# Optimization experiments

Hardware: AMD Instinct MI355X
Metric: run time of the kernel (lower is better)

## Reference

```python
import jax, jax.numpy as jnp
import numpy as np

# Dims: N tokens, top_k K, E experts, d_model D, expert hidden H
N, K, E, D, H = 4096, 2, 8, 1024, 1024


def setup_inputs() -> dict:
    key = jax.random.key(0)
    k1, k2, k3, k4, k5, k6 = jax.random.split(key, 6)
    x = jax.random.normal(k1, (N, D), dtype=jnp.float32)
    expert_indices = jax.random.randint(k2, (N, K), 0, E, dtype=jnp.int32)
    ew = jax.random.uniform(k3, (N, K), dtype=jnp.float32)
    expert_weights = ew / ew.sum(-1, keepdims=True)  # router probs over top-k
    # histogram consistent with expert_indices (computed by the router in the real model)
    batch_size_per_expert = jnp.bincount(expert_indices.reshape(-1), length=E).astype(jnp.int32)
    w1 = jax.random.normal(k4, (E, D, H), dtype=jnp.float32) * (D ** -0.5)
    w3 = jax.random.normal(k5, (E, D, H), dtype=jnp.float32) * (D ** -0.5)
    w2 = jax.random.normal(k6, (E, H, D), dtype=jnp.float32) * (H ** -0.5)
    return {
        "x": x,
        "expert_weights": expert_weights,
        "expert_indices": expert_indices,
        "batch_size_per_expert": batch_size_per_expert,
        "w1": w1,
        "w2": w2,
        "w3": w3,
    }


def reference(x, expert_weights, expert_indices, batch_size_per_expert, w1, w2, w3):
    """Dropless MoE: sort token-copies by expert, grouped-GEMM SwiGLU, unpermute+combine."""
    nk = N * K
    flat_idx = expert_indices.reshape(nk)               # (N*K,)
    order = jnp.argsort(flat_idx)                        # stable sort -> permutation into expert order
    x_perm = x[order // K]                               # (N*K, D) gather source token per copy
    gs = batch_size_per_expert.astype(jnp.int32)         # grouped-GEMM group sizes, sums to N*K
    # per-expert SwiGLU MLP via grouped GEMM (rows of x_perm are contiguous per expert)
    h = jax.nn.silu(jax.lax.ragged_dot(x_perm, w1, gs)) * jax.lax.ragged_dot(x_perm, w3, gs)  # (N*K, H)
    out_perm = jax.lax.ragged_dot(h, w2, gs)             # (N*K, D)
    # unpermute: scatter rows back to original (token, k) order
    out_flat = jnp.zeros_like(x_perm).at[order].set(out_perm)  # (N*K, D)
    # weighted combine over top-k copies
    out = jnp.einsum("nk,nkd->nd", expert_weights, out_flat.reshape(N, K, D))
    return out
```

## Files before the change

kernel.cpp:

```cpp
#include <hip/hip_runtime.h>
#include <hip/hip_bf16.h>
#include <stdint.h>

#define N_TOK   4096
#define TOPK    2
#define N_EXP   8
#define D_MODEL 1024
#define H_DIM   1024
#define NK      (N_TOK * TOPK)
#define MAX_TILES 72

typedef __attribute__((ext_vector_type(8))) short bf16x8;
typedef __attribute__((ext_vector_type(4))) float f32x4;
typedef unsigned short bfbits;

__device__ inline bfbits f2bf_bits(float f) {
  union { float f; unsigned int u; } v; v.f = f;
  unsigned int r = v.u + 0x7FFFu + ((v.u >> 16) & 1u);
  return (bfbits)(r >> 16);
}

__device__ inline void glds16(const bfbits* g, bfbits* l) {
  __builtin_amdgcn_global_load_lds(
      (const __attribute__((address_space(1))) void*)g,
      (__attribute__((address_space(3))) void*)l, 16, 0, 0);
}

__global__ void prep_bucket_kernel(const int* __restrict__ bspe, const int* __restrict__ eidx,
                                   int* __restrict__ meta, int* __restrict__ row_src,
                                   int* __restrict__ pos_of) {
  __shared__ int sm[162];
  __shared__ int scnt[N_EXP];
  int t = threadIdx.x;
  if (t == 0) {
    int acc = 0, nt = 0;
    for (int e = 0; e < N_EXP; e++) {
      sm[e] = acc;
      sm[9 + e] = 0;
      int g = bspe[e];
      for (int tt = 0; tt * 128 < g; tt++) {
        sm[18 + nt] = e;
        sm[90 + nt] = acc + tt * 128;
        nt++;
      }
      acc += g;
    }
    sm[8] = acc;
    sm[17] = nt;
    for (int i = nt; i < MAX_TILES; i++) { sm[18 + i] = 0; sm[90 + i] = 0; }
  }
  if (t < N_EXP) scnt[t] = 0;
  __syncthreads();
  for (int i = t; i < NK; i += 256) {
    int e = eidx[i];
    int p = sm[e] + atomicAdd(&scnt[e], 1);
    row_src[p] = i;
    pos_of[i] = p;
  }
  if (t < 162) meta[t] = sm[t];
}

__global__ void convx_kernel(const float4* __restrict__ x, ushort4* __restrict__ xb) {
  int i = blockIdx.x * 256 + threadIdx.x;
  float4 v = x[i];
  ushort4 o;
  o.x = f2bf_bits(v.x); o.y = f2bf_bits(v.y);
  o.z = f2bf_bits(v.z); o.w = f2bf_bits(v.w);
  xb[i] = o;
}

__global__ void wtrans_kernel(const float* __restrict__ w1, const float* __restrict__ w2,
                              const float* __restrict__ w3,
                              bfbits* __restrict__ w1t, bfbits* __restrict__ w2t,
                              bfbits* __restrict__ w3t) {
  int z = blockIdx.z;
  const size_t MAT = (size_t)1024 * 1024;
  const float* src; bfbits* dst;
  if (z < 8)       { src = w1 + (size_t)z * MAT;        dst = w1t + (size_t)z * MAT; }
  else if (z < 16) { src = w3 + (size_t)(z - 8) * MAT;  dst = w3t + (size_t)(z - 8) * MAT; }
  else             { src = w2 + (size_t)(z - 16) * MAT; dst = w2t + (size_t)(z - 16) * MAT; }
  __shared__ bfbits tl[64][65];
  int tid = threadIdx.x;
  int r0 = blockIdx.y * 64, c0 = blockIdx.x * 64;
  for (int it = 0; it < 4; it++) {
    int r = (tid >> 4) + it * 16;
    int c = (tid & 15) * 4;
    float4 v = *(const float4*)&src[(size_t)(r0 + r) * 1024 + c0 + c];
    tl[r][c + 0] = f2bf_bits(v.x); tl[r][c + 1] = f2bf_bits(v.y);
    tl[r][c + 2] = f2bf_bits(v.z); tl[r][c + 3] = f2bf_bits(v.w);
  }
  __syncthreads();
  for (int it = 0; it < 4; it++) {
    int o = (tid >> 4) + it * 16;
    int r4 = (tid & 15) * 4;
    ushort4 v;
    v.x = tl[r4 + 0][o]; v.y = tl[r4 + 1][o];
    v.z = tl[r4 + 2][o]; v.w = tl[r4 + 3][o];
    *(ushort4*)&dst[(size_t)(c0 + o) * 1024 + r0 + r4] = v;
  }
}

__global__ __launch_bounds__(256, 3) void gemm_swiglu_kernel(
    const bfbits* __restrict__ xb, const bfbits* __restrict__ w1t,
    const bfbits* __restrict__ w3t, const int* __restrict__ row_src,
    const int* __restrict__ meta, bfbits* __restrict__ hb) {
  int nt = meta[17];
  int bt = blockIdx.y;
  if (bt >= nt) return;
  int e = meta[18 + bt];
  int row0 = meta[90 + bt];
  int rows_end = meta[e + 1];
  int n0 = blockIdx.x * 64;

  __shared__ __align__(16) bfbits As[128 * 32];
  __shared__ __align__(16) bfbits B1s[64 * 32];
  __shared__ __align__(16) bfbits B3s[64 * 32];

  int tid = threadIdx.x, lane = tid & 63, wv = tid >> 6;
  int g = (lane & 3) ^ ((lane >> 3) & 3);
  int rlo = lane >> 2;

  const bfbits* gp[4]; bfbits* lp[4];
  for (int j = 0; j < 4; j++) {
    int s = wv * 4 + j;
    if (s < 8) {
      int gr = row0 + s * 16 + rlo;
      int tok = row_src[(gr < rows_end) ? gr : row0] >> 1;
      gp[j] = xb + (size_t)tok * D_MODEL + g * 8;
      lp[j] = As + s * 512;
    } else if (s < 12) {
      int b = s - 8;
      gp[j] = w1t + ((size_t)e * H_DIM + n0 + b * 16 + rlo) * D_MODEL + g * 8;
      lp[j] = B1s + b * 512;
    } else {
      int b = s - 12;
      gp[j] = w3t + ((size_t)e * H_DIM + n0 + b * 16 + rlo) * D_MODEL + g * 8;
      lp[j] = B3s + b * 512;
    }
  }

  const f32x4 fzero = {0.f, 0.f, 0.f, 0.f};
  f32x4 accg[4][2], accu[4][2];
  for (int i = 0; i < 4; i++)
    for (int j = 0; j < 2; j++) { accg[i][j] = fzero; accu[i][j] = fzero; }

  int mw = (wv & 1) * 64, nwv = (wv >> 1) * 32;
  int qd = lane >> 4, lr = lane & 15;
  int slot = (qd ^ ((lr >> 1) & 3)) << 3;

  for (int kk = 0; kk < D_MODEL / 32; kk++) {
    int ko = kk * 32;
    glds16(gp[0] + ko, lp[0]);
    glds16(gp[1] + ko, lp[1]);
    glds16(gp[2] + ko, lp[2]);
    glds16(gp[3] + ko, lp[3]);
    __syncthreads();
    bf16x8 af[4], b1f[2], b3f[2];
    for (int mi = 0; mi < 4; mi++)
      af[mi] = *(const bf16x8*)&As[(mw + mi * 16 + lr) * 32 + slot];
    for (int ni = 0; ni < 2; ni++) {
      b1f[ni] = *(const bf16x8*)&B1s[(nwv + ni * 16 + lr) * 32 + slot];
      b3f[ni] = *(const bf16x8*)&B3s[(nwv + ni * 16 + lr) * 32 + slot];
    }
    for (int mi = 0; mi < 4; mi++)
      for (int ni = 0; ni < 2; ni++) {
        accg[mi][ni] = __builtin_amdgcn_mfma_f32_16x16x32_bf16(af[mi], b1f[ni], accg[mi][ni], 0, 0, 0);
        accu[mi][ni] = __builtin_amdgcn_mfma_f32_16x16x32_bf16(af[mi], b3f[ni], accu[mi][ni], 0, 0, 0);
      }
    __syncthreads();
  }

  for (int mi = 0; mi < 4; mi++) {
    int rbase = row0 + mw + mi * 16 + qd * 4;
    for (int r = 0; r < 4; r++) {
      int grow = rbase + r;
      if (grow < rows_end) {
        for (int ni = 0; ni < 2; ni++) {
          float gg = accg[mi][ni][r], u = accu[mi][ni][r];
          float h = gg / (1.f + __expf(-gg)) * u;
          hb[(size_t)grow * H_DIM + n0 + nwv + ni * 16 + lr] = f2bf_bits(h);
        }
      }
    }
  }
}

__global__ __launch_bounds__(256, 4) void gemm_out_kernel(
    const bfbits* __restrict__ hb, const bfbits* __restrict__ w2t,
    const int* __restrict__ meta, float* __restrict__ out_perm) {
  int nt = meta[17];
  int bt = blockIdx.y;
  if (bt >= nt) return;
  int e = meta[18 + bt];
  int row0 = meta[90 + bt];
  int rows_end = meta[e + 1];
  int n0 = blockIdx.x * 64;

  __shared__ __align__(16) bfbits As[128 * 32];
  __shared__ __align__(16) bfbits Bs[64 * 32];

  int tid = threadIdx.x, lane = tid & 63, wv = tid >> 6;
  int g = (lane & 3) ^ ((lane >> 3) & 3);
  int rlo = lane >> 2;

  const bfbits* gp[3]; bfbits* lp[3];
  for (int j = 0; j < 3; j++) {
    int s = wv * 3 + j;
    if (s < 8) {
      int gr = row0 + s * 16 + rlo;
      int sr = (gr < rows_end) ? gr : row0;
      gp[j] = hb + (size_t)sr * H_DIM + g * 8;
      lp[j] = As + s * 512;
    } else {
      int b = s - 8;
      gp[j] = w2t + ((size_t)e * D_MODEL + n0 + b * 16 + rlo) * H_DIM + g * 8;
      lp[j] = Bs + b * 512;
    }
  }

  const f32x4 fzero = {0.f, 0.f, 0.f, 0.f};
  f32x4 acc[4][2];
  for (int i = 0; i < 4; i++)
    for (int j = 0; j < 2; j++) acc[i][j] = fzero;

  int mw = (wv & 1) * 64, nwv = (wv >> 1) * 32;
  int qd = lane >> 4, lr = lane & 15;
  int slot = (qd ^ ((lr >> 1) & 3)) << 3;

  for (int kk = 0; kk < H_DIM / 32; kk++) {
    int ko = kk * 32;
    glds16(gp[0] + ko, lp[0]);
    glds16(gp[1] + ko, lp[1]);
    glds16(gp[2] + ko, lp[2]);
    __syncthreads();
    bf16x8 af[4], bfr[2];
    for (int mi = 0; mi < 4; mi++)
      af[mi] = *(const bf16x8*)&As[(mw + mi * 16 + lr) * 32 + slot];
    for (int ni = 0; ni < 2; ni++)
      bfr[ni] = *(const bf16x8*)&Bs[(nwv + ni * 16 + lr) * 32 + slot];
    for (int mi = 0; mi < 4; mi++)
      for (int ni = 0; ni < 2; ni++)
        acc[mi][ni] = __builtin_amdgcn_mfma_f32_16x16x32_bf16(af[mi], bfr[ni], acc[mi][ni], 0, 0, 0);
    __syncthreads();
  }

  for (int mi = 0; mi < 4; mi++) {
    int rbase = row0 + mw + mi * 16 + qd * 4;
    for (int r = 0; r < 4; r++) {
      int grow = rbase + r;
      if (grow < rows_end) {
        for (int ni = 0; ni < 2; ni++)
          out_perm[(size_t)grow * D_MODEL + n0 + nwv + ni * 16 + lr] = acc[mi][ni][r];
      }
    }
  }
}

__global__ void combine_kernel(const float4* __restrict__ out_perm,
                               const int* __restrict__ pos_of,
                               const float* __restrict__ ew, float4* __restrict__ out) {
  int i = blockIdx.x * 256 + threadIdx.x;
  int tok = i >> 8;
  int col = i & 255;
  int p0 = pos_of[2 * tok], p1 = pos_of[2 * tok + 1];
  float w0 = ew[2 * tok], w1 = ew[2 * tok + 1];
  float4 a = out_perm[(size_t)p0 * 256 + col];
  float4 b = out_perm[(size_t)p1 * 256 + col];
  float4 o;
  o.x = w0 * a.x + w1 * b.x;
  o.y = w0 * a.y + w1 * b.y;
  o.z = w0 * a.z + w1 * b.z;
  o.w = w0 * a.w + w1 * b.w;
  out[i] = o;
}

extern "C" void kernel_launch(void* const* d_in, const int* in_sizes, int n_in,
                              void* d_out, int out_size, void* d_ws, size_t ws_size,
                              hipStream_t stream) {
  const float* x  = (const float*)d_in[0];
  const float* ew = (const float*)d_in[1];
  const int* eidx = (const int*)d_in[2];
  const int* bspe = (const int*)d_in[3];
  const float* w1 = (const float*)d_in[4];
  const float* w2 = (const float*)d_in[5];
  const float* w3 = (const float*)d_in[6];
  float* out = (float*)d_out;

  char* ws = (char*)d_ws;
  const size_t MB = 1024 * 1024;
  bfbits* w1t   = (bfbits*)(ws);
  bfbits* w3t   = (bfbits*)(ws + 16 * MB);
  bfbits* w2t   = (bfbits*)(ws + 32 * MB);
  bfbits* xb    = (bfbits*)(ws + 48 * MB);
  bfbits* hb    = (bfbits*)(ws + 56 * MB);
  float* out_perm = (float*)(ws);
  int* row_src  = (int*)(ws + 72 * MB);
  int* pos_of   = (int*)(ws + 72 * MB + 32 * 1024);
  int* meta     = (int*)(ws + 72 * MB + 64 * 1024);

  prep_bucket_kernel<<<1, 256, 0, stream>>>(bspe, eidx, meta, row_src, pos_of);
  convx_kernel<<<(N_TOK * D_MODEL / 4) / 256, 256, 0, stream>>>((const float4*)x, (ushort4*)xb);
  wtrans_kernel<<<dim3(16, 16, 24), 256, 0, stream>>>(w1, w2, w3, w1t, w2t, w3t);
  gemm_swiglu_kernel<<<dim3(H_DIM / 64, MAX_TILES), 256, 0, stream>>>(
      xb, w1t, w3t, row_src, meta, hb);
  gemm_out_kernel<<<dim3(D_MODEL / 64, MAX_TILES), 256, 0, stream>>>(
      hb, w2t, meta, out_perm);
  combine_kernel<<<(N_TOK * D_MODEL / 4) / 256, 256, 0, stream>>>(
      (const float4*)out_perm, pos_of, ew, (float4*)out);
}
```

Baseline: 283.1 us.

## Merge prep kernels, double GEMM K-step, and store expert output in bf16

Combines weight transpose, x conversion and bucketing into one launch. Both grouped GEMMs now stage 64-wide K slices with an 8-way XOR swizzle, halving barrier count per K. The per-copy expert output is written as bf16 and widened in the combine kernel, halving that traffic. Tail-row clamping was dropped, so the last tile may read row_src entries beyond valid rows and gather unrelated tokens (masked on store, but indices past NK read adjacent buffer memory).

Measured after the change: 248.6 us. 12.2% less time.

```diff
diff --git a/kernel.cpp b/kernel.cpp
--- a/kernel.cpp
+++ b/kernel.cpp
@@ -19,6 +19,10 @@
   unsigned int r = v.u + 0x7FFFu + ((v.u >> 16) & 1u);
   return (bfbits)(r >> 16);
 }
+__device__ inline float bf2f(unsigned short u) {
+  union { unsigned int u; float f; } v; v.u = ((unsigned int)u) << 16;
+  return v.f;
+}
 
 __device__ inline void glds16(const bfbits* g, bfbits* l) {
   __builtin_amdgcn_global_load_lds(
@@ -26,77 +30,76 @@
       (__attribute__((address_space(3))) void*)l, 16, 0, 0);
 }
 
-__global__ void prep_bucket_kernel(const int* __restrict__ bspe, const int* __restrict__ eidx,
-                                   int* __restrict__ meta, int* __restrict__ row_src,
-                                   int* __restrict__ pos_of) {
-  __shared__ int sm[162];
-  __shared__ int scnt[N_EXP];
-  int t = threadIdx.x;
-  if (t == 0) {
-    int acc = 0, nt = 0;
-    for (int e = 0; e < N_EXP; e++) {
-      sm[e] = acc;
-      sm[9 + e] = 0;
-      int g = bspe[e];
-      for (int tt = 0; tt * 128 < g; tt++) {
-        sm[18 + nt] = e;
-        sm[90 + nt] = acc + tt * 128;
-        nt++;
+__global__ void prepass_kernel(const float* __restrict__ x, const int* __restrict__ eidx,
+                               const int* __restrict__ bspe,
+                               const float* __restrict__ w1, const float* __restrict__ w2,
+                               const float* __restrict__ w3,
+                               bfbits* __restrict__ w1t, bfbits* __restrict__ w2t,
+                               bfbits* __restrict__ w3t, bfbits* __restrict__ xb,
+                               int* __restrict__ meta, int* __restrict__ row_src,
+                               int* __restrict__ pos_of) {
+  int z = blockIdx.z;
+  int tid = threadIdx.x;
+  if (z < 24) {
+    const size_t MAT = (size_t)1024 * 1024;
+    const float* src; bfbits* dst;
+    if (z < 8)       { src = w1 + (size_t)z * MAT;        dst = w1t + (size_t)z * MAT; }
+    else if (z < 16) { src = w3 + (size_t)(z - 8) * MAT;  dst = w3t + (size_t)(z - 8) * MAT; }
+    else             { src = w2 + (size_t)(z - 16) * MAT; dst = w2t + (size_t)(z - 16) * MAT; }
+    __shared__ bfbits tl[64][65];
+    int r0 = blockIdx.y * 64, c0 = blockIdx.x * 64;
+    for (int it = 0; it < 4; it++) {
+      int r = (tid >> 4) + it * 16;
+      int c = (tid & 15) * 4;
+      float4 v = *(const float4*)&src[(size_t)(r0 + r) * 1024 + c0 + c];
+      tl[r][c + 0] = f2bf_bits(v.x); tl[r][c + 1] = f2bf_bits(v.y);
+      tl[r][c + 2] = f2bf_bits(v.z); tl[r][c + 3] = f2bf_bits(v.w);
+    }
+    __syncthreads();
+    for (int it = 0; it < 4; it++) {
+      int o = (tid >> 4) + it * 16;
+      int r4 = (tid & 15) * 4;
+      ushort4 v;
+      v.x = tl[r4 + 0][o]; v.y = tl[r4 + 1][o];
+      v.z = tl[r4 + 2][o]; v.w = tl[r4 + 3][o];
+      *(ushort4*)&dst[(size_t)(c0 + o) * 1024 + r0 + r4] = v;
+    }
+  } else if (z < 40) {
+    int i = ((z - 24) * 256 + blockIdx.y * 16 + blockIdx.x) * 256 + tid;
+    float4 v = ((const float4*)x)[i];
+    ushort4 o;
+    o.x = f2bf_bits(v.x); o.y = f2bf_bits(v.y);
+    o.z = f2bf_bits(v.z); o.w = f2bf_bits(v.w);
+    ((ushort4*)xb)[i] = o;
+  } else {
+    if (blockIdx.x != 0 || blockIdx.y != 0) return;
+    __shared__ int sm[162];
+    __shared__ int scnt[N_EXP];
+    if (tid == 0) {
+      int acc = 0, nt = 0;
+      for (int e = 0; e < N_EXP; e++) {
+        sm[e] = acc;
+        int g = bspe[e];
+        for (int tt = 0; tt * 128 < g; tt++) {
+          sm[18 + nt] = e;
+          sm[90 + nt] = acc + tt * 128;
+          nt++;
+        }
+        acc += g;
       }
-      acc += g;
-    }
-    sm[8] = acc;
-    sm[17] = nt;
-    for (int i = nt; i < MAX_TILES; i++) { sm[18 + i] = 0; sm[90 + i] = 0; }
-  }
-  if (t < N_EXP) scnt[t] = 0;
-  __syncthreads();
-  for (int i = t; i < NK; i += 256) {
-    int e = eidx[i];
-    int p = sm[e] + atomicAdd(&scnt[e], 1);
-    row_src[p] = i;
-    pos_of[i] = p;
-  }
-  if (t < 162) meta[t] = sm[t];
-}
-
-__global__ void convx_kernel(const float4* __restrict__ x, ushort4* __restrict__ xb) {
-  int i = blockIdx.x * 256 + threadIdx.x;
-  float4 v = x[i];
-  ushort4 o;
-  o.x = f2bf_bits(v.x); o.y = f2bf_bits(v.y);
-  o.z = f2bf_bits(v.z); o.w = f2bf_bits(v.w);
-  xb[i] = o;
-}
-
-__global__ void wtrans_kernel(const float* __restrict__ w1, const float* __restrict__ w2,
-                              const float* __restrict__ w3,
-                              bfbits* __restrict__ w1t, bfbits* __restrict__ w2t,
-                              bfbits* __restrict__ w3t) {
-  int z = blockIdx.z;
-  const size_t MAT = (size_t)1024 * 1024;
-  const float* src; bfbits* dst;
-  if (z < 8)       { src = w1 + (size_t)z * MAT;        dst = w1t + (size_t)z * MAT; }
-  else if (z < 16) { src = w3 + (size_t)(z - 8) * MAT;  dst = w3t + (size_t)(z - 8) * MAT; }
-  else             { src = w2 + (size_t)(z - 16) * MAT; dst = w2t + (size_t)(z - 16) * MAT; }
-  __shared__ bfbits tl[64][65];
-  int tid = threadIdx.x;
-  int r0 = blockIdx.y * 64, c0 = blockIdx.x * 64;
-  for (int it = 0; it < 4; it++) {
-    int r = (tid >> 4) + it * 16;
-    int c = (tid & 15) * 4;
-    float4 v = *(const float4*)&src[(size_t)(r0 + r) * 1024 + c0 + c];
-    tl[r][c + 0] = f2bf_bits(v.x); tl[r][c + 1] = f2bf_bits(v.y);
-    tl[r][c + 2] = f2bf_bits(v.z); tl[r][c + 3] = f2bf_bits(v.w);
-  }
-  __syncthreads();
-  for (int it = 0; it < 4; it++) {
-    int o = (tid >> 4) + it * 16;
-    int r4 = (tid & 15) * 4;
-    ushort4 v;
-    v.x = tl[r4 + 0][o]; v.y = tl[r4 + 1][o];
-    v.z = tl[r4 + 2][o]; v.w = tl[r4 + 3][o];
-    *(ushort4*)&dst[(size_t)(c0 + o) * 1024 + r0 + r4] = v;
+      sm[8] = acc;
+      sm[17] = nt;
+      for (int i = nt; i < MAX_TILES; i++) { sm[18 + i] = 0; sm[90 + i] = 0; }
+    }
+    if (tid < N_EXP) scnt[tid] = 0;
+    __syncthreads();
+    for (int i = tid; i < NK; i += 256) {
+      int e = eidx[i];
+      int p = sm[e] + atomicAdd(&scnt[e], 1);
+      row_src[p] = i;
+      pos_of[i] = p;
+    }
+    if (tid < 162) meta[tid] = sm[tid];
   }
 }
 
@@ -112,29 +115,28 @@
   int rows_end = meta[e + 1];
   int n0 = blockIdx.x * 64;
 
-  __shared__ __align__(16) bfbits As[128 * 32];
-  __shared__ __align__(16) bfbits B1s[64 * 32];
-  __shared__ __align__(16) bfbits B3s[64 * 32];
+  __shared__ __align__(16) bfbits As[128 * 64];
+  __shared__ __align__(16) bfbits B1s[64 * 64];
+  __shared__ __align__(16) bfbits B3s[64 * 64];
 
   int tid = threadIdx.x, lane = tid & 63, wv = tid >> 6;
-  int g = (lane & 3) ^ ((lane >> 3) & 3);
-  int rlo = lane >> 2;
-
-  const bfbits* gp[4]; bfbits* lp[4];
-  for (int j = 0; j < 4; j++) {
-    int s = wv * 4 + j;
-    if (s < 8) {
-      int gr = row0 + s * 16 + rlo;
-      int tok = row_src[(gr < rows_end) ? gr : row0] >> 1;
-      gp[j] = xb + (size_t)tok * D_MODEL + g * 8;
+  int r8 = lane >> 3, jl = lane & 7;
+  int jg = jl ^ r8;
+
+  const bfbits* gp[8]; bfbits* lp[8];
+  for (int j = 0; j < 8; j++) {
+    int s = wv * 8 + j;
+    if (s < 16) {
+      int tok = row_src[row0 + s * 8 + r8] >> 1;
+      gp[j] = xb + (size_t)tok * D_MODEL + jg * 8;
       lp[j] = As + s * 512;
-    } else if (s < 12) {
-      int b = s - 8;
-      gp[j] = w1t + ((size_t)e * H_DIM + n0 + b * 16 + rlo) * D_MODEL + g * 8;
+    } else if (s < 24) {
+      int b = s - 16;
+      gp[j] = w1t + ((size_t)e * H_DIM + n0 + b * 8 + r8) * D_MODEL + jg * 8;
       lp[j] = B1s + b * 512;
     } else {
-      int b = s - 12;
-      gp[j] = w3t + ((size_t)e * H_DIM + n0 + b * 16 + rlo) * D_MODEL + g * 8;
+      int b = s - 24;
+      gp[j] = w3t + ((size_t)e * H_DIM + n0 + b * 8 + r8) * D_MODEL + jg * 8;
       lp[j] = B3s + b * 512;
     }
   }
@@ -145,28 +147,27 @@
     for (int j = 0; j < 2; j++) { accg[i][j] = fzero; accu[i][j] = fzero; }
 
   int mw = (wv & 1) * 64, nwv = (wv >> 1) * 32;
-  int qd = lane >> 4, lr = lane & 15;
-  int slot = (qd ^ ((lr >> 1) & 3)) << 3;
-
-  for (int kk = 0; kk < D_MODEL / 32; kk++) {
-    int ko = kk * 32;
-    glds16(gp[0] + ko, lp[0]);
-    glds16(gp[1] + ko, lp[1]);
-    glds16(gp[2] + ko, lp[2]);
-    glds16(gp[3] + ko, lp[3]);
-    __syncthreads();
-    bf16x8 af[4], b1f[2], b3f[2];
-    for (int mi = 0; mi < 4; mi++)
-      af[mi] = *(const bf16x8*)&As[(mw + mi * 16 + lr) * 32 + slot];
-    for (int ni = 0; ni < 2; ni++) {
-      b1f[ni] = *(const bf16x8*)&B1s[(nwv + ni * 16 + lr) * 32 + slot];
-      b3f[ni] = *(const bf16x8*)&B3s[(nwv + ni * 16 + lr) * 32 + slot];
-    }
-    for (int mi = 0; mi < 4; mi++)
+  int qd = lane >> 4, lr = lane & 15, lr7 = lr & 7;
+
+  for (int kk = 0; kk < D_MODEL / 64; kk++) {
+    int ko = kk * 64;
+    for (int j = 0; j < 8; j++) glds16(gp[j] + ko, lp[j]);
+    __syncthreads();
+    for (int ks = 0; ks < 2; ks++) {
+      int sb = ((ks * 4 + qd) ^ lr7) << 3;
+      bf16x8 af[4], b1f[2], b3f[2];
+      for (int mi = 0; mi < 4; mi++)
+        af[mi] = *(const bf16x8*)&As[(mw + mi * 16 + lr) * 64 + sb];
       for (int ni = 0; ni < 2; ni++) {
-        accg[mi][ni] = __builtin_amdgcn_mfma_f32_16x16x32_bf16(af[mi], b1f[ni], accg[mi][ni], 0, 0, 0);
-        accu[mi][ni] = __builtin_amdgcn_mfma_f32_16x16x32_bf16(af[mi], b3f[ni], accu[mi][ni], 0, 0, 0);
+        b1f[ni] = *(const bf16x8*)&B1s[(nwv + ni * 16 + lr) * 64 + sb];
+        b3f[ni] = *(const bf16x8*)&B3s[(nwv + ni * 16 + lr) * 64 + sb];
       }
+      for (int mi = 0; mi < 4; mi++)
+        for (int ni = 0; ni < 2; ni++) {
+          accg[mi][ni] = __builtin_amdgcn_mfma_f32_16x16x32_bf16(af[mi], b1f[ni], accg[mi][ni], 0, 0, 0);
+          accu[mi][ni] = __builtin_amdgcn_mfma_f32_16x16x32_bf16(af[mi], b3f[ni], accu[mi][ni], 0, 0, 0);
+        }
+    }
     __syncthreads();
   }
 
@@ -187,7 +188,7 @@
 
 __global__ __launch_bounds__(256, 4) void gemm_out_kernel(
     const bfbits* __restrict__ hb, const bfbits* __restrict__ w2t,
-    const int* __restrict__ meta, float* __restrict__ out_perm) {
+    const int* __restrict__ meta, bfbits* __restrict__ out_perm) {
   int nt = meta[17];
   int bt = blockIdx.y;
   if (bt >= nt) return;
@@ -196,24 +197,22 @@
   int rows_end = meta[e + 1];
   int n0 = blockIdx.x * 64;
 
-  __shared__ __align__(16) bfbits As[128 * 32];
-  __shared__ __align__(16) bfbits Bs[64 * 32];
+  __shared__ __align__(16) bfbits As[128 * 64];
+  __shared__ __align__(16) bfbits Bs[64 * 64];
 
   int tid = threadIdx.x, lane = tid & 63, wv = tid >> 6;
-  int g = (lane & 3) ^ ((lane >> 3) & 3);
-  int rlo = lane >> 2;
-
-  const bfbits* gp[3]; bfbits* lp[3];
-  for (int j = 0; j < 3; j++) {
-    int s = wv * 3 + j;
-    if (s < 8) {
-      int gr = row0 + s * 16 + rlo;
-      int sr = (gr < rows_end) ? gr : row0;
-      gp[j] = hb + (size_t)sr * H_DIM + g * 8;
+  int r8 = lane >> 3, jl = lane & 7;
+  int jg = jl ^ r8;
+
+  const bfbits* gp[6]; bfbits* lp[6];
+  for (int j = 0; j < 6; j++) {
+    int s = wv * 6 + j;
+    if (s < 16) {
+      gp[j] = hb + (size_t)(row0 + s * 8 + r8) * H_DIM + jg * 8;
       lp[j] = As + s * 512;
     } else {
-      int b = s - 8;
-      gp[j] = w2t + ((size_t)e * D_MODEL + n0 + b * 16 + rlo) * H_DIM + g * 8;
+      int b = s - 16;
+      gp[j] = w2t + ((size_t)e * D_MODEL + n0 + b * 8 + r8) * H_DIM + jg * 8;
       lp[j] = Bs + b * 512;
     }
   }
@@ -224,23 +223,23 @@
     for (int j = 0; j < 2; j++) acc[i][j] = fzero;
 
   int mw = (wv & 1) * 64, nwv = (wv >> 1) * 32;
-  int qd = lane >> 4, lr = lane & 15;
-  int slot = (qd ^ ((lr >> 1) & 3)) << 3;
-
-  for (int kk = 0; kk < H_DIM / 32; kk++) {
-    int ko = kk * 32;
-    glds16(gp[0] + ko, lp[0]);
-    glds16(gp[1] + ko, lp[1]);
-    glds16(gp[2] + ko, lp[2]);
-    __syncthreads();
-    bf16x8 af[4], bfr[2];
-    for (int mi = 0; mi < 4; mi++)
-      af[mi] = *(const bf16x8*)&As[(mw + mi * 16 + lr) * 32 + slot];
-    for (int ni = 0; ni < 2; ni++)
-      bfr[ni] = *(const bf16x8*)&Bs[(nwv + ni * 16 + lr) * 32 + slot];
-    for (int mi = 0; mi < 4; mi++)
+  int qd = lane >> 4, lr = lane & 15, lr7 = lr & 7;
+
+  for (int kk = 0; kk < H_DIM / 64; kk++) {
+    int ko = kk * 64;
+    for (int j = 0; j < 6; j++) glds16(gp[j] + ko, lp[j]);
+    __syncthreads();
+    for (int ks = 0; ks < 2; ks++) {
+      int sb = ((ks * 4 + qd) ^ lr7) << 3;
+      bf16x8 af[4], bfr[2];
+      for (int mi = 0; mi < 4; mi++)
+        af[mi] = *(const bf16x8*)&As[(mw + mi * 16 + lr) * 64 + sb];
       for (int ni = 0; ni < 2; ni++)
-        acc[mi][ni] = __builtin_amdgcn_mfma_f32_16x16x32_bf16(af[mi], bfr[ni], acc[mi][ni], 0, 0, 0);
+        bfr[ni] = *(const bf16x8*)&Bs[(nwv + ni * 16 + lr) * 64 + sb];
+      for (int mi = 0; mi < 4; mi++)
+        for (int ni = 0; ni < 2; ni++)
+          acc[mi][ni] = __builtin_amdgcn_mfma_f32_16x16x32_bf16(af[mi], bfr[ni], acc[mi][ni], 0, 0, 0);
+    }
     __syncthreads();
   }
 
@@ -250,13 +249,13 @@
       int grow = rbase + r;
       if (grow < rows_end) {
         for (int ni = 0; ni < 2; ni++)
-          out_perm[(size_t)grow * D_MODEL + n0 + nwv + ni * 16 + lr] = acc[mi][ni][r];
+          out_perm[(size_t)grow * D_MODEL + n0 + nwv + ni * 16 + lr] = f2bf_bits(acc[mi][ni][r]);
       }
     }
   }
 }
 
-__global__ void combine_kernel(const float4* __restrict__ out_perm,
+__global__ void combine_kernel(const ushort4* __restrict__ out_perm,
                                const int* __restrict__ pos_of,
                                const float* __restrict__ ew, float4* __restrict__ out) {
   int i = blockIdx.x * 256 + threadIdx.x;
@@ -264,13 +263,13 @@
   int col = i & 255;
   int p0 = pos_of[2 * tok], p1 = pos_of[2 * tok + 1];
   float w0 = ew[2 * tok], w1 = ew[2 * tok + 1];
-  float4 a = out_perm[(size_t)p0 * 256 + col];
-  float4 b = out_perm[(size_t)p1 * 256 + col];
+  ushort4 a = out_perm[(size_t)p0 * 256 + col];
+  ushort4 b = out_perm[(size_t)p1 * 256 + col];
   float4 o;
-  o.x = w0 * a.x + w1 * b.x;
-  o.y = w0 * a.y + w1 * b.y;
-  o.z = w0 * a.z + w1 * b.z;
-  o.w = w0 * a.w + w1 * b.w;
+  o.x = w0 * bf2f(a.x) + w1 * bf2f(b.x);
+  o.y = w0 * bf2f(a.y) + w1 * bf2f(b.y);
+  o.z = w0 * bf2f(a.z) + w1 * bf2f(b.z);
+  o.w = w0 * bf2f(a.w) + w1 * bf2f(b.w);
   out[i] = o;
 }
 
@@ -293,18 +292,17 @@
   bfbits* w2t   = (bfbits*)(ws + 32 * MB);
   bfbits* xb    = (bfbits*)(ws + 48 * MB);
   bfbits* hb    = (bfbits*)(ws + 56 * MB);
-  float* out_perm = (float*)(ws);
+  bfbits* out_perm = (bfbits*)(ws);
   int* row_src  = (int*)(ws + 72 * MB);
   int* pos_of   = (int*)(ws + 72 * MB + 32 * 1024);
   int* meta     = (int*)(ws + 72 * MB + 64 * 1024);
 
-  prep_bucket_kernel<<<1, 256, 0, stream>>>(bspe, eidx, meta, row_src, pos_of);
-  convx_kernel<<<(N_TOK * D_MODEL / 4) / 256, 256, 0, stream>>>((const float4*)x, (ushort4*)xb);
-  wtrans_kernel<<<dim3(16, 16, 24), 256, 0, stream>>>(w1, w2, w3, w1t, w2t, w3t);
+  prepass_kernel<<<dim3(16, 16, 41), 256, 0, stream>>>(
+      x, eidx, bspe, w1, w2, w3, w1t, w2t, w3t, xb, meta, row_src, pos_of);
   gemm_swiglu_kernel<<<dim3(H_DIM / 64, MAX_TILES), 256, 0, stream>>>(
       xb, w1t, w3t, row_src, meta, hb);
   gemm_out_kernel<<<dim3(D_MODEL / 64, MAX_TILES), 256, 0, stream>>>(
       hb, w2t, meta, out_perm);
   combine_kernel<<<(N_TOK * D_MODEL / 4) / 256, 256, 0, stream>>>(
-      (const float4*)out_perm, pos_of, ew, (float4*)out);
-}
+      (const ushort4*)out_perm, pos_of, ew, (float4*)out);
+}
```
